# Performance work log

Measured on AMD Instinct MI355X. Metric: run time of the kernel, lower is better.

## Reference

```python
import jax, jax.numpy as jnp
import numpy as np

B, S, H, I, E, TOP_K = 2, 2048, 1024, 2048, 8, 2


def setup_inputs() -> dict:
    key = jax.random.key(0)
    k1, k2, k3, k4, k5 = jax.random.split(key, 5)
    scale_h = 1.0 / np.sqrt(H)
    scale_i = 1.0 / np.sqrt(I)
    return {
        "hidden_states": jax.random.normal(k1, (B, S, H), dtype=jnp.float32),
        "router_w": jax.random.normal(k2, (H, E), dtype=jnp.float32) * scale_h,
        "gate_w": jax.random.normal(k3, (E, H, I), dtype=jnp.float32) * scale_h,
        "up_w": jax.random.normal(k4, (E, H, I), dtype=jnp.float32) * scale_h,
        "out_w": jax.random.normal(k5, (E, I, H), dtype=jnp.float32) * scale_i,
    }


def reference(hidden_states, router_w, gate_w, up_w, out_w):
    b, s, h = hidden_states.shape
    x = hidden_states.reshape(-1, h)  # [T, H], T = B*S

    # Router: logits -> softmax -> top-k -> renormalize -> dense routing matrix
    router_logits = x @ router_w  # [T, E]
    router_probs = jax.nn.softmax(router_logits, axis=-1)
    top_p, top_i = jax.lax.top_k(router_probs, TOP_K)  # [T, K]
    top_p = top_p / jnp.sum(top_p, axis=-1, keepdims=True)
    one_hot = jax.nn.one_hot(top_i, E, dtype=top_p.dtype)  # [T, K, E]
    routing_full = jnp.sum(one_hot * top_p[..., None], axis=1)  # [T, E]
    routing_full = routing_full.T  # [E, T]

    # Dense all-expert FFN (SwiGLU), as in the original batched einsum form
    gate = jnp.einsum("th,ehm->etm", x, gate_w)  # [E, T, I]
    gate = jax.nn.silu(gate)
    intermediate = jnp.einsum("th,ehm->etm", x, up_w)  # [E, T, I]
    hidden = intermediate * gate
    expert_out = jnp.einsum("eti,eih->eth", hidden, out_w)  # [E, T, H]

    # Weighted combine over experts
    out = jnp.sum(expert_out * routing_full[:, :, None], axis=0)  # [T, H]
    out = out.reshape(b, s, h)
    return out, router_logits
```

## Files before the change

kernel.cpp:

```cpp
#include <hip/hip_runtime.h>
#include <hip/hip_bf16.h>
#include <stdint.h>

#define TT 4096
#define HH 1024
#define II 2048
#define EE 8
#define RB 16
#define NRB (TT / RB)
#define CSTRIDE 32
#define NTRB (2 * 2048)
#define NZB 256

typedef short bf16x8 __attribute__((ext_vector_type(8)));
typedef float f32x4 __attribute__((ext_vector_type(4)));

__device__ __forceinline__ unsigned short f2bf(float f) {
  unsigned u = __float_as_uint(f);
  u += 0x7FFF + ((u >> 16) & 1);
  return (unsigned short)(u >> 16);
}

__device__ __forceinline__ void gl_lds16(const void* g, void* l) {
  auto gp = reinterpret_cast<const __attribute__((address_space(1))) unsigned int*>(
      reinterpret_cast<uintptr_t>(g));
  auto lp = reinterpret_cast<__attribute__((address_space(3))) unsigned int*>(
      reinterpret_cast<uintptr_t>(l));
  __builtin_amdgcn_global_load_lds(gp, lp, 16, 0, 0);
}

__device__ __forceinline__ void transpose_tile_wide(const float* __restrict__ in,
                                                    unsigned short* __restrict__ out,
                                                    int M, int N, int mB, int nB,
                                                    unsigned int* tl, int tid) {
  union F4 { float4 v; float f[4]; };
  int n4 = tid & 31;
  int mph = tid >> 5;
  F4 a[4], bq[4];
  const float* base = in + (size_t)mB * N + nB + n4 * 4;
#pragma unroll
  for (int it = 0; it < 4; ++it) {
    const float* p = base + (size_t)(2 * (mph + it * 8)) * N;
    a[it].v = *(const float4*)p;
    bq[it].v = *(const float4*)(p + N);
  }
#pragma unroll
  for (int it = 0; it < 4; ++it) {
    int mp = mph + it * 8;
#pragma unroll
    for (int i = 0; i < 4; ++i) {
      int n = n4 * 4 + i;
      unsigned v = (unsigned)f2bf(a[it].f[i]) | ((unsigned)f2bf(bq[it].f[i]) << 16);
      tl[n * 32 + ((mp + (n >> 2) + (n & 3)) & 31)] = v;
    }
  }
  __syncthreads();
  int md = tid & 7;
  int nr = tid >> 3;
#pragma unroll
  for (int it = 0; it < 4; ++it) {
    int n = nr + it * 32;
    int rot = (n >> 2) + (n & 3);
    unsigned vv[4];
#pragma unroll
    for (int k = 0; k < 4; ++k)
      vv[k] = tl[n * 32 + ((md * 4 + k + rot) & 31)];
    *(uint4*)(out + (size_t)(nB + n) * M + mB + md * 8) = make_uint4(vv[0], vv[1], vv[2], vv[3]);
  }
}

__global__ __launch_bounds__(256, 4)
void front_kernel(const float* __restrict__ x, const float* __restrict__ rw,
                  const float* __restrict__ gw, const float* __restrict__ uw,
                  float* __restrict__ logits_out, unsigned short* __restrict__ xb,
                  unsigned short* __restrict__ gwt, unsigned short* __restrict__ uwt,
                  int* __restrict__ gcnt, int2* __restrict__ ttop,
                  float* __restrict__ outz) {
  __shared__ unsigned int tl[4096];
  int b = blockIdx.x;
  int tid = threadIdx.x;

  if (b >= NRB + NTRB) {
    int zb = b - NRB - NTRB;
    float4* o = (float4*)outz + (size_t)zb * 4096 + tid;
    float4 z = make_float4(0.f, 0.f, 0.f, 0.f);
#pragma unroll
    for (int k = 0; k < 16; ++k) o[k * 256] = z;
    return;
  }

  if (b >= NRB) {
    int idx = b - NRB;
    int which = idx >> 11;
    int r = idx & 2047;
    int e = r >> 8;
    int tile = r & 255;
    int bx = tile & 15, by = tile >> 4;
    const float* in = (which ? uw : gw) + (size_t)e * HH * II;
    unsigned short* o = (which ? uwt : gwt) + (size_t)e * HH * II;
    transpose_tile_wide(in, o, HH, II, by * 64, bx * 128, tl, tid);
    return;
  }

  __shared__ int bcnt[EE];
  int wave = tid >> 6, lane = tid & 63;
  if (tid < EE) bcnt[tid] = 0;
  __syncthreads();
  int t0 = b * RB;

  for (int sub = 0; sub < RB / 4; ++sub) {
    int li = sub * 4 + wave;
    int t = t0 + li;
    float acc[EE];
#pragma unroll
    for (int e = 0; e < EE; ++e) acc[e] = 0.f;
#pragma unroll
    for (int j = 0; j < 4; ++j) {
      int h = j * 256 + lane * 4;
      union F4 { float4 v; float f[4]; } xv;
      xv.v = *(const float4*)(x + (size_t)t * HH + h);
      union { unsigned short s[4]; uint2 v; } pk;
#pragma unroll
      for (int i = 0; i < 4; ++i) pk.s[i] = f2bf(xv.f[i]);
      *(uint2*)(xb + (size_t)t * HH + h) = pk.v;
#pragma unroll
      for (int i = 0; i < 4; ++i) {
        const float4* r4 = (const float4*)(rw + (h + i) * EE);
        float4 r0 = r4[0], r1 = r4[1];
        float xs = xv.f[i];
        acc[0] += xs * r0.x; acc[1] += xs * r0.y; acc[2] += xs * r0.z; acc[3] += xs * r0.w;
        acc[4] += xs * r1.x; acc[5] += xs * r1.y; acc[6] += xs * r1.z; acc[7] += xs * r1.w;
      }
    }
#pragma unroll
    for (int e = 0; e < EE; ++e)
#pragma unroll
      for (int off = 32; off; off >>= 1) acc[e] += __shfl_down(acc[e], off);
    if (lane == 0) {
      float4* lo = (float4*)(logits_out + (size_t)t * EE);
      lo[0] = make_float4(acc[0], acc[1], acc[2], acc[3]);
      lo[1] = make_float4(acc[4], acc[5], acc[6], acc[7]);
      int e0 = 0; float b0 = acc[0];
#pragma unroll
      for (int e = 1; e < EE; ++e) if (acc[e] > b0) { b0 = acc[e]; e0 = e; }
      int e1 = -1; float b1 = -3.4e38f;
#pragma unroll
      for (int e = 0; e < EE; ++e) if (e != e0 && acc[e] > b1) { b1 = acc[e]; e1 = e; }
      float w0 = 1.f / (1.f + __expf(b1 - b0));
      int lp0 = atomicAdd(&bcnt[e0], 1);
      int lp1 = atomicAdd(&bcnt[e1], 1);
      ttop[t] = make_int2(e0 | (e1 << 3) | (lp0 << 6) | (lp1 << 11), __float_as_int(w0));
    }
  }
  __syncthreads();
  if (tid < EE) gcnt[b * EE + tid] = bcnt[tid];
}

__global__ void scatter_kernel(const int* __restrict__ gcnt, const int2* __restrict__ ttop,
                               int* __restrict__ cnt, int* __restrict__ list,
                               float* __restrict__ rwt) {
  __shared__ int raw[NRB * EE];
  __shared__ int base[NRB][EE];
  int tid = threadIdx.x;
  for (int i = tid; i < NRB * EE; i += 256) raw[i] = gcnt[i];
  __syncthreads();
  if (tid < EE) {
    int s = 0;
    for (int b = 0; b < NRB; ++b) { base[b][tid] = s; s += raw[b * EE + tid]; }
    if (blockIdx.x == 0) cnt[tid * CSTRIDE] = s;
  }
  __syncthreads();
  int t = blockIdx.x * 256 + tid;
  int2 ti = ttop[t];
  int v = ti.x;
  float w0 = __int_as_float(ti.y);
  int e0 = v & 7, e1 = (v >> 3) & 7, lp0 = (v >> 6) & 31, lp1 = (v >> 11) & 31;
  int b = t >> 4;
  int p0 = base[b][e0] + lp0;
  int p1 = base[b][e1] + lp1;
  list[e0 * TT + p0] = t;
  list[e1 * TT + p1] = t;
  rwt[e0 * TT + p0] = w0;
  rwt[e1 * TT + p1] = 1.f - w0;
}

__launch_bounds__(256, 4)
__global__ void gemm1_kernel(const unsigned short* __restrict__ xb,
                             const unsigned short* __restrict__ gwt,
                             const unsigned short* __restrict__ uwt,
                             const float* __restrict__ ow, unsigned short* __restrict__ owt,
                             unsigned short* __restrict__ hidden,
                             const int* __restrict__ cnt, const int* __restrict__ list) {
  __shared__ __align__(16) unsigned short smem[16384];
  __shared__ int stok[128];
  int tid = threadIdx.x;
  int e = blockIdx.z;

  if (blockIdx.y >= 32) {
    int tile = (blockIdx.y - 32) * 32 + blockIdx.x;
    int bx = tile & 7, by = tile >> 3;
    transpose_tile_wide(ow + (size_t)e * II * HH, owt + (size_t)e * II * HH,
                        II, HH, by * 64, bx * 128, (unsigned int*)smem, tid);
    return;
  }

  int cn = cnt[e * CSTRIDE];
  int hb0 = 0;
  for (int i = 0; i < EE; ++i) hb0 += (i < e) ? cnt[i * CSTRIDE] : 0;
  int mBase = blockIdx.y * 128;
  if (mBase >= cn) return;
  int nBase = blockIdx.x * 64;

  int wave = tid >> 6, lane = tid & 63;
  if (tid < 128) {
    int g = mBase + tid;
    stok[tid] = list[e * TT + (g < cn ? g : cn - 1)];
  }
  __syncthreads();

  const char* gaddr[4];
  int lofs[4];
#pragma unroll
  for (int j = 0; j < 4; ++j) {
    int c = wave * 256 + j * 64 + lane;
    const char* g;
    if (c < 512) {
      int r = c >> 2, kc = (c & 3) ^ ((r >> 1) & 3);
      g = (const char*)xb + (size_t)stok[r] * (HH * 2) + kc * 16;
    } else if (c < 768) {
      int cc = c - 512, r = cc >> 2, kc = (cc & 3) ^ ((r >> 1) & 3);
      g = (const char*)gwt + ((size_t)e * II + nBase + r) * (HH * 2) + kc * 16;
    } else {
      int cc = c - 768, r = cc >> 2, kc = (cc & 3) ^ ((r >> 1) & 3);
      g = (const char*)uwt + ((size_t)e * II + nBase + r) * (HH * 2) + kc * 16;
    }
    gaddr[j] = g;
    lofs[j] = c * 16;
  }

  int q = lane >> 4, m16 = lane & 15;
  int wr = wave & 1, wc = wave >> 1;
  int faddrA[4], faddrBg[2], faddrBu[2];
#pragma unroll
  for (int mi = 0; mi < 4; ++mi) {
    int R = wr * 64 + mi * 16 + m16;
    faddrA[mi] = (R * 4 + (q ^ ((R >> 1) & 3))) * 16;
  }
#pragma unroll
  for (int ni = 0; ni < 2; ++ni) {
    int n = wc * 32 + ni * 16 + m16;
    faddrBg[ni] = (512 + n * 4 + (q ^ ((n >> 1) & 3))) * 16;
    faddrBu[ni] = (768 + n * 4 + (q ^ ((n >> 1) & 3))) * 16;
  }

  f32x4 zero4 = {0.f, 0.f, 0.f, 0.f};
  f32x4 accG[4][2], accU[4][2];
#pragma unroll
  for (int mi = 0; mi < 4; ++mi)
#pragma unroll
    for (int ni = 0; ni < 2; ++ni) { accG[mi][ni] = zero4; accU[mi][ni] = zero4; }

  char* smemc = (char*)smem;
#pragma unroll
  for (int j = 0; j < 4; ++j) {
    gl_lds16(gaddr[j], smemc + lofs[j]);
    gaddr[j] += 64;
  }
  __syncthreads();

  const int NK = HH / 32;
  for (int kt = 0; kt < NK; ++kt) {
    int cur = kt & 1;
    if (kt + 1 < NK) {
#pragma unroll
      for (int j = 0; j < 4; ++j) {
        gl_lds16(gaddr[j], smemc + (cur ^ 1) * 16384 + lofs[j]);
        gaddr[j] += 64;
      }
    }
    const char* sb = smemc + cur * 16384;
    bf16x8 aF[4], bG[2], bU[2];
#pragma unroll
    for (int mi = 0; mi < 4; ++mi) aF[mi] = *(const bf16x8*)(sb + faddrA[mi]);
#pragma unroll
    for (int ni = 0; ni < 2; ++ni) {
      bG[ni] = *(const bf16x8*)(sb + faddrBg[ni]);
      bU[ni] = *(const bf16x8*)(sb + faddrBu[ni]);
    }
#pragma unroll
    for (int mi = 0; mi < 4; ++mi)
#pragma unroll
      for (int ni = 0; ni < 2; ++ni) {
        accG[mi][ni] = __builtin_amdgcn_mfma_f32_16x16x32_bf16(aF[mi], bG[ni], accG[mi][ni], 0, 0, 0);
        accU[mi][ni] = __builtin_amdgcn_mfma_f32_16x16x32_bf16(aF[mi], bU[ni], accU[mi][ni], 0, 0, 0);
      }
    __syncthreads();
  }

  int hb = hb0 + mBase;
  int rowsValid = cn - mBase; if (rowsValid > 128) rowsValid = 128;
#pragma unroll
  for (int mi = 0; mi < 4; ++mi)
#pragma unroll
    for (int ni = 0; ni < 2; ++ni)
#pragma unroll
      for (int r = 0; r < 4; ++r) {
        int row = wr * 64 + mi * 16 + q * 4 + r;
        if (row < rowsValid) {
          float g = accG[mi][ni][r], u = accU[mi][ni][r];
          float h = g / (1.f + __expf(-g)) * u;
          hidden[(size_t)(hb + row) * II + nBase + wc * 32 + ni * 16 + m16] = f2bf(h);
        }
      }
}

__launch_bounds__(256, 4)
__global__ void gemm2_kernel(const unsigned short* __restrict__ hidden,
                             const unsigned short* __restrict__ owt,
                             float* __restrict__ out,
                             const int* __restrict__ cnt, const int* __restrict__ list,
                             const float* __restrict__ rwt) {
  int e = blockIdx.z;
  int cn = cnt[e * CSTRIDE];
  int hb0 = 0;
  for (int i = 0; i < EE; ++i) hb0 += (i < e) ? cnt[i * CSTRIDE] : 0;
  int mBase = blockIdx.y * 128;
  if (mBase >= cn) return;
  int nBase = blockIdx.x * 128;

  __shared__ __align__(16) unsigned short smem[16384];
  __shared__ int stok[128];
  __shared__ float swt[128];

  int tid = threadIdx.x, wave = tid >> 6, lane = tid & 63;
  int hb = hb0 + mBase;
  if (tid < 128) {
    int g = mBase + tid;
    int gi = g < cn ? g : cn - 1;
    stok[tid] = list[e * TT + gi];
    swt[tid] = rwt[e * TT + gi];
  }
  const char* gaddr[4];
  int lofs[4];
#pragma unroll
  for (int j = 0; j < 4; ++j) {
    int c = wave * 256 + j * 64 + lane;
    const char* g;
    if (c < 512) {
      int r = c >> 2, kc = (c & 3) ^ ((r >> 1) & 3);
      g = (const char*)hidden + (size_t)(hb + r) * (II * 2) + kc * 16;
    } else {
      int cc = c - 512, r = cc >> 2, kc = (cc & 3) ^ ((r >> 1) & 3);
      g = (const char*)owt + ((size_t)e * HH + nBase + r) * (II * 2) + kc * 16;
    }
    gaddr[j] = g;
    lofs[j] = c * 16;
  }

  int q = lane >> 4, m16 = lane & 15;
  int wr = wave & 1, wc = wave >> 1;
  int faddrA[4], faddrB[4];
#pragma unroll
  for (int mi = 0; mi < 4; ++mi) {
    int R = wr * 64 + mi * 16 + m16;
    faddrA[mi] = (R * 4 + (q ^ ((R >> 1) & 3))) * 16;
  }
#pragma unroll
  for (int ni = 0; ni < 4; ++ni) {
    int n = wc * 64 + ni * 16 + m16;
    faddrB[ni] = (512 + n * 4 + (q ^ ((n >> 1) & 3))) * 16;
  }

  f32x4 zero4 = {0.f, 0.f, 0.f, 0.f};
  f32x4 acc[4][4];
#pragma unroll
  for (int mi = 0; mi < 4; ++mi)
#pragma unroll
    for (int ni = 0; ni < 4; ++ni) acc[mi][ni] = zero4;

  char* smemc = (char*)smem;
#pragma unroll
  for (int j = 0; j < 4; ++j) {
    gl_lds16(gaddr[j], smemc + lofs[j]);
    gaddr[j] += 64;
  }
  __syncthreads();

  const int NK = II / 32;
  for (int kt = 0; kt < NK; ++kt) {
    int cur = kt & 1;
    if (kt + 1 < NK) {
#pragma unroll
      for (int j = 0; j < 4; ++j) {
        gl_lds16(gaddr[j], smemc + (cur ^ 1) * 16384 + lofs[j]);
        gaddr[j] += 64;
      }
    }
    const char* sb = smemc + cur * 16384;
    bf16x8 aF[4], bF[4];
#pragma unroll
    for (int mi = 0; mi < 4; ++mi) aF[mi] = *(const bf16x8*)(sb + faddrA[mi]);
#pragma unroll
    for (int ni = 0; ni < 4; ++ni) bF[ni] = *(const bf16x8*)(sb + faddrB[ni]);
#pragma unroll
    for (int mi = 0; mi < 4; ++mi)
#pragma unroll
      for (int ni = 0; ni < 4; ++ni)
        acc[mi][ni] = __builtin_amdgcn_mfma_f32_16x16x32_bf16(aF[mi], bF[ni], acc[mi][ni], 0, 0, 0);
    __syncthreads();
  }

  int rowsValid = cn - mBase; if (rowsValid > 128) rowsValid = 128;
#pragma unroll
  for (int mi = 0; mi < 4; ++mi)
#pragma unroll
    for (int r = 0; r < 4; ++r) {
      int row = wr * 64 + mi * 16 + q * 4 + r;
      if (row < rowsValid) {
        int t = stok[row];
        float w = swt[row];
        float* orow = out + (size_t)t * HH + nBase + wc * 64 + m16;
#pragma unroll
        for (int ni = 0; ni < 4; ++ni)
          atomicAdd(orow + ni * 16, w * acc[mi][ni][r]);
      }
    }
}

extern "C" void kernel_launch(void* const* d_in, const int* in_sizes, int n_in,
                              void* d_out, int out_size, void* d_ws, size_t ws_size,
                              hipStream_t stream) {
  (void)in_sizes; (void)n_in; (void)out_size; (void)ws_size;
  const float* x  = (const float*)d_in[0];
  const float* rw = (const float*)d_in[1];
  const float* gw = (const float*)d_in[2];
  const float* uw = (const float*)d_in[3];
  const float* ow = (const float*)d_in[4];
  float* out = (float*)d_out;
  float* logits = out + (size_t)TT * HH;

  char* ws = (char*)d_ws;
  size_t o = 0;
  auto alloc = [&](size_t bytes) {
    char* p = ws + o;
    o += (bytes + 255) & ~(size_t)255;
    return p;
  };
  unsigned short* xb  = (unsigned short*)alloc((size_t)TT * HH * 2);
  unsigned short* gwt = (unsigned short*)alloc((size_t)EE * II * HH * 2);
  unsigned short* uwt = (unsigned short*)alloc((size_t)EE * II * HH * 2);
  unsigned short* owt = (unsigned short*)alloc((size_t)EE * HH * II * 2);
  unsigned short* hidden = (unsigned short*)alloc((size_t)(2 * TT + 128) * II * 2);
  int*    cnt   = (int*)alloc(EE * CSTRIDE * 4);
  int*    list  = (int*)alloc((size_t)EE * TT * 4);
  float*  rwt   = (float*)alloc((size_t)EE * TT * 4);
  int*    gcnt  = (int*)alloc((size_t)NRB * EE * 4);
  int2*   ttop  = (int2*)alloc((size_t)TT * 8);

  front_kernel<<<NRB + NTRB + NZB, 256, 0, stream>>>(x, rw, gw, uw, logits, xb, gwt, uwt,
                                                     gcnt, ttop, out);
  scatter_kernel<<<TT / 256, 256, 0, stream>>>(gcnt, ttop, cnt, list, rwt);
  gemm1_kernel<<<dim3(32, 40, EE), 256, 0, stream>>>(xb, gwt, uwt, ow, owt, hidden, cnt, list);
  gemm2_kernel<<<dim3(HH / 128, TT / 128, EE), 256, 0, stream>>>(hidden, owt, out, cnt, list, rwt);
}
```

Baseline: 420.5 us.

## Split gemm2 K dimension in two and swap grid axes for token-major order

gemm2 now splits the 2048-long reduction into two halves, selected by blockIdx.z, to double the number of active blocks. Each iteration loads a 64-wide K tile into a single LDS buffer with an 8-way XOR swizzle, replacing the previous double-buffered 32-wide tiles. Both GEMM kernels swap blockIdx.x and blockIdx.y so adjacent blocks walk token tiles, which changes the order weights and activations are reused. The cost is twice as many float atomics into the output and the loss of load/compute overlap from double buffering.

```diff
diff --git a/kernel.cpp b/kernel.cpp
--- a/kernel.cpp
+++ b/kernel.cpp
@@ -207,9 +207,9 @@
   int cn = cnt[e * CSTRIDE];
   int hb0 = 0;
   for (int i = 0; i < EE; ++i) hb0 += (i < e) ? cnt[i * CSTRIDE] : 0;
-  int mBase = blockIdx.y * 128;
+  int mBase = blockIdx.x * 128;
   if (mBase >= cn) return;
-  int nBase = blockIdx.x * 64;
+  int nBase = blockIdx.y * 64;
 
   int wave = tid >> 6, lane = tid & 63;
   if (tid < 128) {
@@ -320,13 +320,14 @@
                              float* __restrict__ out,
                              const int* __restrict__ cnt, const int* __restrict__ list,
                              const float* __restrict__ rwt) {
-  int e = blockIdx.z;
+  int e = blockIdx.z >> 1;
+  int kh = blockIdx.z & 1;
   int cn = cnt[e * CSTRIDE];
   int hb0 = 0;
   for (int i = 0; i < EE; ++i) hb0 += (i < e) ? cnt[i * CSTRIDE] : 0;
-  int mBase = blockIdx.y * 128;
+  int mBase = blockIdx.x * 128;
   if (mBase >= cn) return;
-  int nBase = blockIdx.x * 128;
+  int nBase = blockIdx.y * 128;
 
   __shared__ __align__(16) unsigned short smem[16384];
   __shared__ int stok[128];
@@ -340,35 +341,39 @@
     stok[tid] = list[e * TT + gi];
     swt[tid] = rwt[e * TT + gi];
   }
-  const char* gaddr[4];
-  int lofs[4];
-#pragma unroll
-  for (int j = 0; j < 4; ++j) {
-    int c = wave * 256 + j * 64 + lane;
+  __syncthreads();
+
+  const char* gaddr[8];
+#pragma unroll
+  for (int j = 0; j < 8; ++j) {
+    int c = wave * 512 + j * 64 + lane;
     const char* g;
-    if (c < 512) {
-      int r = c >> 2, kc = (c & 3) ^ ((r >> 1) & 3);
-      g = (const char*)hidden + (size_t)(hb + r) * (II * 2) + kc * 16;
+    if (c < 1024) {
+      int r = c >> 3, sl = (c & 7) ^ (r & 7);
+      g = (const char*)hidden + (size_t)(hb + r) * (II * 2) + kh * 2048 + sl * 16;
     } else {
-      int cc = c - 512, r = cc >> 2, kc = (cc & 3) ^ ((r >> 1) & 3);
-      g = (const char*)owt + ((size_t)e * HH + nBase + r) * (II * 2) + kc * 16;
+      int cc = c - 1024, r = cc >> 3, sl = (cc & 7) ^ (r & 7);
+      g = (const char*)owt + ((size_t)e * HH + nBase + r) * (II * 2) + kh * 2048 + sl * 16;
     }
     gaddr[j] = g;
-    lofs[j] = c * 16;
   }
 
   int q = lane >> 4, m16 = lane & 15;
   int wr = wave & 1, wc = wave >> 1;
-  int faddrA[4], faddrB[4];
+  int faddrA[4][2], faddrB[4][2];
 #pragma unroll
   for (int mi = 0; mi < 4; ++mi) {
     int R = wr * 64 + mi * 16 + m16;
-    faddrA[mi] = (R * 4 + (q ^ ((R >> 1) & 3))) * 16;
+#pragma unroll
+    for (int h = 0; h < 2; ++h)
+      faddrA[mi][h] = (R * 8 + ((h * 4 + q) ^ (R & 7))) * 16;
   }
 #pragma unroll
   for (int ni = 0; ni < 4; ++ni) {
     int n = wc * 64 + ni * 16 + m16;
-    faddrB[ni] = (512 + n * 4 + (q ^ ((n >> 1) & 3))) * 16;
+#pragma unroll
+    for (int h = 0; h < 2; ++h)
+      faddrB[ni][h] = (1024 + n * 8 + ((h * 4 + q) ^ (n & 7))) * 16;
   }
 
   f32x4 zero4 = {0.f, 0.f, 0.f, 0.f};
@@ -378,36 +383,29 @@
 #pragma unroll
     for (int ni = 0; ni < 4; ++ni) acc[mi][ni] = zero4;
 
-  char* smemc = (char*)smem;
-#pragma unroll
-  for (int j = 0; j < 4; ++j) {
-    gl_lds16(gaddr[j], smemc + lofs[j]);
-    gaddr[j] += 64;
-  }
-  __syncthreads();
-
-  const int NK = II / 32;
+  const char* smemc = (const char*)smem;
+  const int NK = 1024 / 64;
   for (int kt = 0; kt < NK; ++kt) {
-    int cur = kt & 1;
-    if (kt + 1 < NK) {
-#pragma unroll
-      for (int j = 0; j < 4; ++j) {
-        gl_lds16(gaddr[j], smemc + (cur ^ 1) * 16384 + lofs[j]);
-        gaddr[j] += 64;
-      }
-    }
-    const char* sb = smemc + cur * 16384;
-    bf16x8 aF[4], bF[4];
-#pragma unroll
-    for (int mi = 0; mi < 4; ++mi) aF[mi] = *(const bf16x8*)(sb + faddrA[mi]);
-#pragma unroll
-    for (int ni = 0; ni < 4; ++ni) bF[ni] = *(const bf16x8*)(sb + faddrB[ni]);
-#pragma unroll
-    for (int mi = 0; mi < 4; ++mi)
-#pragma unroll
-      for (int ni = 0; ni < 4; ++ni)
-        acc[mi][ni] = __builtin_amdgcn_mfma_f32_16x16x32_bf16(aF[mi], bF[ni], acc[mi][ni], 0, 0, 0);
     __syncthreads();
+#pragma unroll
+    for (int j = 0; j < 8; ++j) {
+      gl_lds16(gaddr[j], (char*)smem + (size_t)(wave * 512 + j * 64) * 16);
+      gaddr[j] += 128;
+    }
+    __syncthreads();
+#pragma unroll
+    for (int h = 0; h < 2; ++h) {
+      bf16x8 aF[4], bF[4];
+#pragma unroll
+      for (int mi = 0; mi < 4; ++mi) aF[mi] = *(const bf16x8*)(smemc + faddrA[mi][h]);
+#pragma unroll
+      for (int ni = 0; ni < 4; ++ni) bF[ni] = *(const bf16x8*)(smemc + faddrB[ni][h]);
+#pragma unroll
+      for (int mi = 0; mi < 4; ++mi)
+#pragma unroll
+        for (int ni = 0; ni < 4; ++ni)
+          acc[mi][ni] = __builtin_amdgcn_mfma_f32_16x16x32_bf16(aF[mi], bF[ni], acc[mi][ni], 0, 0, 0);
+    }
   }
 
   int rowsValid = cn - mBase; if (rowsValid > 128) rowsValid = 128;
@@ -461,5 +459,5 @@
                                                      gcnt, ttop, out);
   scatter_kernel<<<TT / 256, 256, 0, stream>>>(gcnt, ttop, cnt, list, rwt);
   gemm1_kernel<<<dim3(32, 40, EE), 256, 0, stream>>>(xb, gwt, uwt, ow, owt, hidden, cnt, list);
-  gemm2_kernel<<<dim3(HH / 128, TT / 128, EE), 256, 0, stream>>>(hidden, owt, out, cnt, list, rwt);
-}
+  gemm2_kernel<<<dim3(TT / 128, HH / 128, EE * 2), 256, 0, stream>>>(hidden, owt, out, cnt, list, rwt);
+}
```

After: 741.0 us. +76.2%, slower.
